# Kernel optimization log

Measured on AMD Instinct MI355X. Metric: run time of the kernel, lower is better.

Reference implementation:

```python
import jax, jax.numpy as jnp
import numpy as np

B, CIN, C, H, T = 8, 64, 64, 62, 400
S = 32              # StateSpaceLayer state_dim default
MID = max(1, C // 16)  # ChannelAttention reduction=16


def _dwconv(x, w, pad):
    # x [B,C,H,W], w [C,1,kh,kw], depthwise conv
    return jax.lax.conv_general_dilated(
        x, w, (1, 1), pad,
        dimension_numbers=('NCHW', 'OIHW', 'NCHW'),
        feature_group_count=x.shape[1])


def _pw(x, w):  # 1x1 conv, w [O,C]
    return jnp.einsum('bchw,oc->bohw', x, w)


def _bn(x, g, b):  # eval-mode BatchNorm with running mean=0, var=1 folded into affine
    return x * g[None, :, None, None] + b[None, :, None, None]


def _chan_attn(x, w1, w2):
    # AdaptiveAvg/MaxPool(1) -> shared MLP -> sigmoid gate
    avg = x.mean(axis=(2, 3))
    mx = x.max(axis=(2, 3))
    fc = lambda v: jax.nn.relu(v @ w1.T) @ w2.T  # Linear weights are [out,in]
    a = jax.nn.sigmoid(fc(avg) + fc(mx))
    return x * a[:, :, None, None]


def _spat_attn(x, w):
    avg = x.mean(axis=1, keepdims=True)
    mx = x.max(axis=1, keepdims=True)
    comb = jnp.concatenate([avg, mx], axis=1)  # [B,2,H,W]
    a = jax.nn.sigmoid(jax.lax.conv_general_dilated(
        comb, w, (1, 1), ((3, 3), (3, 3)),
        dimension_numbers=('NCHW', 'OIHW', 'NCHW')))
    return x * a


def _ssm(x, A, Bv, Cm, D, ln_g, ln_b):
    # Faithful to torch: raw reshape [B,C,H,T] -> [B*H, C, T] (row-major, same as torch)
    b, c, h, t = x.shape
    xs = x.reshape(b * h, c, t)
    seq = jnp.moveaxis(xs, 2, 0)  # [T, N, C]

    def step(state, inp):
        state = state @ A.T + Bv               # state = state A^T + B
        out = jax.nn.gelu(state @ Cm + inp * D, approximate=False)
        return state, out

    init = jnp.zeros((b * h, A.shape[0]), x.dtype)
    _, outs = jax.lax.scan(step, init, seq)    # outs [T, N, C]
    out = jnp.moveaxis(outs, 0, 2).reshape(b, c, h, t)
    out = x + out  # residual (dropout p=0)
    # LayerNorm over channel dim
    y = jnp.moveaxis(out, 1, -1)  # [B,H,T,C]
    mu = y.mean(-1, keepdims=True)
    var = ((y - mu) ** 2).mean(-1, keepdims=True)
    y = (y - mu) / jnp.sqrt(var + 1e-5) * ln_g + ln_b
    return jnp.moveaxis(y, -1, 1)


def _half(x, dwdw, dwpw, dwg, dwb, caw1, caw2, saw,
          d1dw, d1pw, d1g, d1b, A, Bv, Cm, D, lng, lnb):
    pad5 = ((2, 2), (2, 2))
    b1 = jax.nn.relu(_bn(_pw(_dwconv(x, dwdw[0], pad5), dwpw[0]), dwg[0], dwb[0]))
    b2 = jax.nn.relu(_bn(_pw(_dwconv(x, dwdw[1], pad5), dwpw[1]), dwg[1], dwb[1]))
    cb = b1 * _chan_attn(b1, caw1, caw2)       # note: x * ChannelAttention(x) as in source
    cb = _bn(_pw(_dwconv(cb, d1dw, ((0, 0), (1, 1))), d1pw), d1g, d1b)
    cb = jax.nn.sigmoid(cb)
    sb = jax.nn.sigmoid(b2 * _spat_attn(b2, saw))
    return _ssm(cb, A, Bv, Cm, D, lng, lnb) * sb


def setup_inputs() -> dict:
    key = jax.random.key(0)
    ks = jax.random.split(key, 16)
    n = lambda k, shp, s=0.1: jax.random.normal(k, shp, dtype=jnp.float32) * s
    return {
        'x': jax.random.normal(ks[0], (B, CIN, H, T), dtype=jnp.float32),
        'in_w': n(ks[1], (C, CIN)),
        'dw2d_dw': n(ks[2], (2, 2, C, 1, 5, 5)),
        'dw2d_pw': n(ks[3], (2, 2, C, C)),
        'dw2d_g': jnp.ones((2, 2, C), jnp.float32),
        'dw2d_b': jnp.zeros((2, 2, C), jnp.float32),
        'ca_w1': n(ks[4], (2, MID, C)),
        'ca_w2': n(ks[5], (2, C, MID)),
        'sa_w': n(ks[6], (2, 1, 2, 7, 7)),
        'dw1d_dw': n(ks[7], (2, C, 1, 1, 3)),
        'dw1d_pw': n(ks[8], (2, C, C)),
        'dw1d_g': jnp.ones((2, C), jnp.float32),
        'dw1d_b': jnp.zeros((2, C), jnp.float32),
        'ssm_A': n(ks[9], (2, S, S)),
        'ssm_B': n(ks[10], (2, S)),
        'ssm_C': n(ks[11], (2, S, C)),
        'ssm_D': n(ks[12], (2, C)),
        'ln_g': jnp.ones((2, C), jnp.float32),
        'ln_b': jnp.zeros((2, C), jnp.float32),
        'out_w': n(ks[13], (C, C)),
        'out_g': jnp.ones((C,), jnp.float32),
        'out_b': jnp.zeros((C,), jnp.float32),
    }


def reference(x, in_w, dw2d_dw, dw2d_pw, dw2d_g, dw2d_b, ca_w1, ca_w2, sa_w,
              dw1d_dw, dw1d_pw, dw1d_g, dw1d_b, ssm_A, ssm_B, ssm_C, ssm_D,
              ln_g, ln_b, out_w, out_g, out_b):
    h = _pw(x, in_w)
    o = _half(h, dw2d_dw[0], dw2d_pw[0], dw2d_g[0], dw2d_b[0], ca_w1[0], ca_w2[0],
              sa_w[0], dw1d_dw[0], dw1d_pw[0], dw1d_g[0], dw1d_b[0],
              ssm_A[0], ssm_B[0], ssm_C[0], ssm_D[0], ln_g[0], ln_b[0])
    o = o[..., ::-1]  # flip time axis
    o = _half(o, dw2d_dw[1], dw2d_pw[1], dw2d_g[1], dw2d_b[1], ca_w1[1], ca_w2[1],
              sa_w[1], dw1d_dw[1], dw1d_pw[1], dw1d_g[1], dw1d_b[1],
              ssm_A[1], ssm_B[1], ssm_C[1], ssm_D[1], ln_g[1], ln_b[1])
    o = o[..., ::-1]
    return jax.nn.relu(_bn(_pw(o, out_w), out_g, out_b))
```

## Files before the change

### kernel.cpp

```cpp
#include <hip/hip_runtime.h>
#include <math.h>

#define DI __device__ __forceinline__

constexpr int B_ = 8, C_ = 64, H_ = 62, T_ = 400, S_ = 32;
constexpr int HT   = H_ * T_;
constexpr int CHT  = C_ * HT;
constexpr int NPOS = B_ * HT;
constexpr int NTOT = B_ * CHT;

typedef __attribute__((ext_vector_type(8))) short short8;
typedef __attribute__((ext_vector_type(4))) float float4v;
typedef unsigned short bh;

DI float sigmoidf_(float x) { return 1.f / (1.f + expf(-x)); }
DI float gelu_(float x) { return 0.5f * x * (1.f + erff(x * 0.70710678118654752f)); }

template<int ACT> DI float act_(float v) {
  if (ACT == 1) return fmaxf(v, 0.f);
  if (ACT == 2) return sigmoidf_(v);
  return v;
}

DI bh f2b(float f) {
  unsigned int u = __float_as_uint(f);
  u += 0x7FFFu + ((u >> 16) & 1u);
  return (bh)(u >> 16);
}
DI float b2f(bh u) { return __uint_as_float(((unsigned int)u) << 16); }
DI unsigned int pk2(float a, float b) {
  return (unsigned int)f2b(a) | ((unsigned int)f2b(b) << 16);
}

__global__ __launch_bounds__(256) void prep(const float* __restrict__ in_w,
    const float* __restrict__ dwpw, const float* __restrict__ dwg,
    const float* __restrict__ d1pw, const float* __restrict__ d1g,
    const float* __restrict__ outw, const float* __restrict__ outg,
    bh* __restrict__ wf) {
  int idx = blockIdx.x * 256 + threadIdx.x;
  int lane = idx & 63, kc = (idx >> 6) & 1, w = (idx >> 7) & 3, slot = idx >> 9;
  const float* src; const float* g;
  switch (slot) {
    case 0: src = in_w;            g = nullptr;      break;
    case 1: src = dwpw + 0 * 4096; g = dwg + 0 * 64; break;
    case 2: src = dwpw + 1 * 4096; g = dwg + 1 * 64; break;
    case 3: src = d1pw + 0 * 4096; g = d1g + 0 * 64; break;
    case 4: src = dwpw + 2 * 4096; g = dwg + 2 * 64; break;
    case 5: src = dwpw + 3 * 4096; g = dwg + 3 * 64; break;
    case 6: src = d1pw + 1 * 4096; g = d1g + 1 * 64; break;
    default: src = outw;           g = outg;         break;
  }
  int o = w * 16 + (lane & 15);
  float gv = g ? g[o] : 1.f;
  unsigned int pack[4];
  #pragma unroll
  for (int h = 0; h < 4; ++h) {
    int c = kc * 32 + (lane >> 4) * 8 + h * 2;
    pack[h] = pk2(src[o * 64 + c] * gv, src[o * 64 + c + 1] * gv);
  }
  *(uint4*)&wf[idx * 8] = make_uint4(pack[0], pack[1], pack[2], pack[3]);
}

template<int ACT, bool REV, bool SPAT, bool DW13, bool INF32, bool OUTF32>
__global__ __launch_bounds__(256) void pwk(const void* __restrict__ in_,
    const bh* __restrict__ wf, const float* __restrict__ bb,
    const float* __restrict__ ac, const float* __restrict__ w3,
    void* __restrict__ out_, float* __restrict__ comb) {
  __shared__ bh Xb[128 * 72];
  const int tid = threadIdx.x;
  const int lane = tid & 63;
  const int wv = tid >> 6;
  const int p0 = blockIdx.x * 128;
  {
    const int ps = (tid & 31) * 4;
    const int cs = (tid >> 5) * 8;
    const int p4 = p0 + ps;
    const int b = p4 / HT, ht = p4 - b * HT;
    const int row = ht / T_, t0 = ht - row * T_;
    float xv[8][4];
    if constexpr (INF32) {
      const float* rp0 = (const float*)in_ + b * CHT + row * T_;
      #pragma unroll
      for (int cj = 0; cj < 8; ++cj) {
        const float* rp = rp0 + (cs + cj) * HT;
        if constexpr (REV) {
          float4 u = *(const float4*)&rp[T_ - 4 - t0];
          xv[cj][0] = u.w; xv[cj][1] = u.z; xv[cj][2] = u.y; xv[cj][3] = u.x;
        } else {
          float4 u = *(const float4*)&rp[t0];
          xv[cj][0] = u.x; xv[cj][1] = u.y; xv[cj][2] = u.z; xv[cj][3] = u.w;
        }
      }
    } else if constexpr (DW13) {
      const bh* rp0 = (const bh*)in_ + b * CHT + row * T_;
      #pragma unroll
      for (int cj = 0; cj < 8; ++cj) {
        const int c = cs + cj;
        const bh* rp = rp0 + c * HT;
        ushort4 u = *(const ushort4*)&rp[t0];
        float x0 = b2f(u.x), x1 = b2f(u.y), x2 = b2f(u.z), x3 = b2f(u.w);
        float xm = (t0 > 0)      ? b2f(rp[t0 - 1]) : 0.f;
        float xp = (t0 < T_ - 4) ? b2f(rp[t0 + 4]) : 0.f;
        float s0 = xm * xm, s1 = x0 * x0, s2 = x1 * x1;
        float s3 = x2 * x2, s4 = x3 * x3, s5 = xp * xp;
        float acv = ac[b * 64 + c];
        float c0 = w3[c * 3 + 0] * acv, c1 = w3[c * 3 + 1] * acv,
              c2 = w3[c * 3 + 2] * acv;
        xv[cj][0] = c0 * s0 + c1 * s1 + c2 * s2;
        xv[cj][1] = c0 * s1 + c1 * s2 + c2 * s3;
        xv[cj][2] = c0 * s2 + c1 * s3 + c2 * s4;
        xv[cj][3] = c0 * s3 + c1 * s4 + c2 * s5;
      }
    } else {
      const bh* rp0 = (const bh*)in_ + b * CHT + row * T_;
      #pragma unroll
      for (int cj = 0; cj < 8; ++cj) {
        const bh* rp = rp0 + (cs + cj) * HT;
        ushort4 u;
        if constexpr (REV) {
          u = *(const ushort4*)&rp[T_ - 4 - t0];
          xv[cj][0] = b2f(u.w); xv[cj][1] = b2f(u.z);
          xv[cj][2] = b2f(u.y); xv[cj][3] = b2f(u.x);
        } else {
          u = *(const ushort4*)&rp[t0];
          xv[cj][0] = b2f(u.x); xv[cj][1] = b2f(u.y);
          xv[cj][2] = b2f(u.z); xv[cj][3] = b2f(u.w);
        }
      }
    }
    #pragma unroll
    for (int pi = 0; pi < 4; ++pi) {
      int r = ps + pi;
      int col = cs ^ (((r >> 2) & 7) << 3);
      uint4 w4;
      w4.x = pk2(xv[0][pi], xv[1][pi]);
      w4.y = pk2(xv[2][pi], xv[3][pi]);
      w4.z = pk2(xv[4][pi], xv[5][pi]);
      w4.w = pk2(xv[6][pi], xv[7][pi]);
      *(uint4*)&Xb[r * 72 + col] = w4;
    }
  }
  short8 af0 = *(const short8*)(wf + ((wv * 2 + 0) * 64 + lane) * 8);
  short8 af1 = *(const short8*)(wf + ((wv * 2 + 1) * 64 + lane) * 8);
  const int m4 = (lane >> 4) * 4;
  float binit[4];
  #pragma unroll
  for (int j = 0; j < 4; ++j) binit[j] = bb ? bb[wv * 16 + m4 + j] : 0.f;
  __syncthreads();
  float4v acc[8];
  #pragma unroll
  for (int nt = 0; nt < 8; ++nt) { acc[nt][0] = acc[nt][1] = acc[nt][2] = acc[nt][3] = 0.f; }
  #pragma unroll
  for (int nt = 0; nt < 8; ++nt) {
    int r = nt * 16 + (lane & 15);
    int sw = ((r >> 2) & 7) << 3;
    int cb0 = ((lane >> 4) * 8) ^ sw;
    int cb1 = (32 + (lane >> 4) * 8) ^ sw;
    short8 b0 = *(const short8*)&Xb[r * 72 + cb0];
    short8 b1 = *(const short8*)&Xb[r * 72 + cb1];
    acc[nt] = __builtin_amdgcn_mfma_f32_16x16x32_bf16(af0, b0, acc[nt], 0, 0, 0);
    acc[nt] = __builtin_amdgcn_mfma_f32_16x16x32_bf16(af1, b1, acc[nt], 0, 0, 0);
  }
  float psum[8], pmaxv[8];
  #pragma unroll
  for (int nt = 0; nt < 8; ++nt) {
    int n = nt * 16 + (lane & 15);
    int p = p0 + n;
    int b = p / HT, ht = p - b * HT;
    float s = 0.f, m = -3.4e38f;
    if constexpr (OUTF32) {
      float* op = (float*)out_ + b * CHT + ht + (wv * 16 + m4) * HT;
      #pragma unroll
      for (int j = 0; j < 4; ++j) {
        float r = act_<ACT>(acc[nt][j] + binit[j]);
        op[j * HT] = r;
        if constexpr (SPAT) { s += r; m = fmaxf(m, r); }
      }
    } else {
      bh* op = (bh*)out_ + b * CHT + ht + (wv * 16 + m4) * HT;
      #pragma unroll
      for (int j = 0; j < 4; ++j) {
        float r = act_<ACT>(acc[nt][j] + binit[j]);
        op[j * HT] = f2b(r);
        if constexpr (SPAT) { s += r; m = fmaxf(m, r); }
      }
    }
    if constexpr (SPAT) {
      s += __shfl_xor(s, 16); s += __shfl_xor(s, 32);
      m = fmaxf(m, __shfl_xor(m, 16)); m = fmaxf(m, __shfl_xor(m, 32));
      psum[nt] = s; pmaxv[nt] = m;
    }
  }
  if constexpr (SPAT) {
    __shared__ float redS[4][128], redM[4][128];
    if (lane < 16) {
      #pragma unroll
      for (int nt = 0; nt < 8; ++nt) {
        redS[wv][nt * 16 + lane] = psum[nt];
        redM[wv][nt * 16 + lane] = pmaxv[nt];
      }
    }
    __syncthreads();
    if (tid < 128) {
      float s = redS[0][tid] + redS[1][tid] + redS[2][tid] + redS[3][tid];
      float m = fmaxf(fmaxf(redM[0][tid], redM[1][tid]),
                      fmaxf(redM[2][tid], redM[3][tid]));
      int pp = p0 + tid;
      int b2 = pp / HT, ht2 = pp - b2 * HT;
      comb[b2 * 2 * HT + ht2] = s * (1.f / 64.f);
      comb[b2 * 2 * HT + HT + ht2] = m;
    }
  }
}

__global__ __launch_bounds__(256) void dw5dual(const float* __restrict__ in,
    const float* __restrict__ w0_, const float* __restrict__ w1_,
    bh* __restrict__ out0, bh* __restrict__ out1) {
  const int bc = blockIdx.y;
  const int c = bc & 63;
  int task = blockIdx.x * 256 + threadIdx.x;
  if (task >= 62 * 25) return;
  int h = task / 25;
  int t0 = (task - h * 25) << 4;
  const float* base = in + (size_t)bc * HT;
  const float* wp0 = w0_ + c * 25;
  const float* wp1 = w1_ + c * 25;
  float acc0[16], acc1[16];
  #pragma unroll
  for (int j = 0; j < 16; ++j) { acc0[j] = 0.f; acc1[j] = 0.f; }
  const bool fast = (t0 >= 4) && (t0 <= 380);
  #pragma unroll 1
  for (int u = 0; u < 5; ++u) {
    int hh = h + u - 2;
    if (hh < 0 || hh >= H_) continue;
    const float* row = base + hh * T_;
    float win[24];
    if (fast) {
      #pragma unroll
      for (int j = 0; j < 6; ++j)
        *(float4*)&win[4 * j] = *(const float4*)&row[t0 - 4 + 4 * j];
    } else {
      #pragma unroll
      for (int k = 0; k < 24; ++k) {
        int tt = t0 - 4 + k;
        win[k] = (tt >= 0 && tt < T_) ? row[tt] : 0.f;
      }
    }
    #pragma unroll
    for (int v = 0; v < 5; ++v) {
      float wa = wp0[u * 5 + v];
      float wb = wp1[u * 5 + v];
      #pragma unroll
      for (int j = 0; j < 16; ++j) {
        float x = win[j + v + 2];
        acc0[j] += wa * x;
        acc1[j] += wb * x;
      }
    }
  }
  unsigned int pk0[8], pk1[8];
  #pragma unroll
  for (int j = 0; j < 8; ++j) {
    pk0[j] = pk2(acc0[2 * j], acc0[2 * j + 1]);
    pk1[j] = pk2(acc1[2 * j], acc1[2 * j + 1]);
  }
  bh* o0 = out0 + (size_t)bc * HT + h * T_ + t0;
  bh* o1 = out1 + (size_t)bc * HT + h * T_ + t0;
  *(uint4*)&o0[0] = make_uint4(pk0[0], pk0[1], pk0[2], pk0[3]);
  *(uint4*)&o0[8] = make_uint4(pk0[4], pk0[5], pk0[6], pk0[7]);
  *(uint4*)&o1[0] = make_uint4(pk1[0], pk1[1], pk1[2], pk1[3]);
  *(uint4*)&o1[8] = make_uint4(pk1[4], pk1[5], pk1[6], pk1[7]);
}

__global__ __launch_bounds__(256) void chanred(const bh* __restrict__ in,
    float* __restrict__ sum_, float* __restrict__ max_) {
  int bc = blockIdx.x >> 1, hf = blockIdx.x & 1;
  const bh* base = in + (size_t)bc * HT + hf * (HT / 2);
  float s = 0.f, m = -3.4e38f;
  for (int i = threadIdx.x * 2; i < HT / 2; i += 512) {
    ushort2 q = *(const ushort2*)&base[i];
    float v0 = b2f(q.x), v1 = b2f(q.y);
    s += v0 + v1; m = fmaxf(m, fmaxf(v0, v1));
  }
  #pragma unroll
  for (int off = 32; off > 0; off >>= 1) {
    s += __shfl_down(s, off);
    m = fmaxf(m, __shfl_down(m, off));
  }
  __shared__ float ss[4], sm[4];
  int wv = threadIdx.x >> 6;
  if ((threadIdx.x & 63) == 0) { ss[wv] = s; sm[wv] = m; }
  __syncthreads();
  if (threadIdx.x == 0) {
    float S = ss[0] + ss[1] + ss[2] + ss[3];
    float M = fmaxf(fmaxf(sm[0], sm[1]), fmaxf(sm[2], sm[3]));
    sum_[hf * 512 + bc] = S;
    max_[hf * 512 + bc] = M;
  }
}

__global__ __launch_bounds__(512) void cafc(const float* __restrict__ cs,
    const float* __restrict__ cm, const float* __restrict__ w1,
    const float* __restrict__ w2, float* __restrict__ ac) {
  __shared__ float sa[512], sx[512], hsum[8][4];
  int tid = threadIdx.x;
  sa[tid] = (cs[tid] + cs[512 + tid]) * (1.f / HT);
  sx[tid] = fmaxf(cm[tid], cm[512 + tid]);
  __syncthreads();
  if (tid < 32) {
    int b = tid >> 2, m = tid & 3;
    float s1 = 0.f, s2 = 0.f;
    #pragma unroll
    for (int cc = 0; cc < 64; ++cc) {
      float wv = w1[m * 64 + cc];
      s1 += sa[b * 64 + cc] * wv;
      s2 += sx[b * 64 + cc] * wv;
    }
    hsum[b][m] = fmaxf(s1, 0.f) + fmaxf(s2, 0.f);
  }
  __syncthreads();
  int b = tid >> 6, cc = tid & 63;
  float f = 0.f;
  #pragma unroll
  for (int m = 0; m < 4; ++m) f += hsum[b][m] * w2[cc * 4 + m];
  ac[tid] = sigmoidf_(f);
}

__global__ __launch_bounds__(256) void conv7(const float* __restrict__ comb,
    const float* __restrict__ w, float* __restrict__ as_) {
  __shared__ float sm[2][8][408];
  __shared__ float sw[98];
  const int b = blockIdx.x / 31, hp = blockIdx.x % 31;
  const int h0 = hp * 2;
  const float* cb0 = comb + b * 2 * HT;
  const int tid = threadIdx.x;
  if (tid < 98) sw[tid] = w[tid];
  for (int e = tid; e < 2 * 8 * 408; e += 256) {
    int ci = e / 3264, rem = e - ci * 3264;
    int r = rem / 408, tt = rem - r * 408;
    int hh = h0 - 3 + r, t = tt - 4;
    float v = 0.f;
    if (hh >= 0 && hh < H_ && t >= 0 && t < T_) v = cb0[ci * HT + hh * T_ + t];
    sm[ci][r][tt] = v;
  }
  __syncthreads();
  for (int o = tid; o < 800; o += 256) {
    int oh = o / 400, ot = o - oh * 400;
    float acc = 0.f;
    #pragma unroll
    for (int ci = 0; ci < 2; ++ci)
      #pragma unroll
      for (int u = 0; u < 7; ++u)
        #pragma unroll
        for (int v = 0; v < 7; ++v)
          acc += sw[ci * 49 + u * 7 + v] * sm[ci][oh + u][ot + v + 1];
    as_[b * HT + (h0 + oh) * T_ + ot] = sigmoidf_(acc);
  }
}

__global__ __launch_bounds__(1024) void ssmctA(const float* __restrict__ A_,
    const float* __restrict__ Bv_, float* __restrict__ Pg, float* __restrict__ qg) {
  const int hf = blockIdx.x;
  const float* A = A_ + hf * 1024;
  const float* Bv = Bv_ + hf * 32;
  __shared__ float Pbuf[2][32 * 33];
  __shared__ float qbuf[2][32];
  const int tid = threadIdx.x;
  float* Pc = Pbuf[0]; float* Pn = Pbuf[1];
  float* qc = qbuf[0]; float* qn = qbuf[1];
  Pc[(tid >> 5) * 33 + (tid & 31)] = A[tid];
  if (tid < 32) qc[tid] = Bv[tid];
  __syncthreads();
  for (int i = 0; i < 9; ++i) {
    Pg[(hf * 9 + i) * 1024 + tid] = Pc[(tid >> 5) * 33 + (tid & 31)];
    if (tid < 32) qg[(hf * 9 + i) * 32 + tid] = qc[tid];
    if (i == 8) break;
    const int r = tid >> 5, cc = tid & 31;
    float s0 = 0.f, s1 = 0.f, s2 = 0.f, s3 = 0.f;
    #pragma unroll
    for (int k = 0; k < 32; k += 4) {
      s0 += Pc[r * 33 + k + 0] * Pc[(k + 0) * 33 + cc];
      s1 += Pc[r * 33 + k + 1] * Pc[(k + 1) * 33 + cc];
      s2 += Pc[r * 33 + k + 2] * Pc[(k + 2) * 33 + cc];
      s3 += Pc[r * 33 + k + 3] * Pc[(k + 3) * 33 + cc];
    }
    float qv = 0.f;
    if (tid < 32) {
      float a0 = 0.f, a1 = 0.f;
      #pragma unroll
      for (int k = 0; k < 32; k += 2) {
        a0 += Pc[tid * 33 + k] * qc[k];
        a1 += Pc[tid * 33 + k + 1] * qc[k + 1];
      }
      qv = qc[tid] + a0 + a1;
    }
    Pn[r * 33 + cc] = s0 + s1 + s2 + s3;
    if (tid < 32) qn[tid] = qv;
    __syncthreads();
    float* tp = Pc; Pc = Pn; Pn = tp;
    float* tq = qc; qc = qn; qn = tq;
  }
}

__global__ __launch_bounds__(1024) void ssmctB(const float* __restrict__ Pg,
    const float* __restrict__ qg, const float* __restrict__ Cm_,
    float* __restrict__ ct) {
  const int hf = blockIdx.y;
  __shared__ float P[9][32][33];
  __shared__ float q[9][32];
  __shared__ float Cs[32 * 64];
  __shared__ float st[32][33];
  const int tid = threadIdx.x;
  #pragma unroll
  for (int i = 0; i < 9; ++i) {
    int rem = tid;
    P[i][rem >> 5][rem & 31] = Pg[(hf * 9 + i) * 1024 + rem];
  }
  if (tid < 9 * 32) q[tid >> 5][tid & 31] = qg[hf * 9 * 32 + tid];
  for (int e = tid; e < 2048; e += 1024) Cs[e] = Cm_[hf * 2048 + e];
  __syncthreads();
  const int grp = tid >> 5, j = tid & 31;
  const int tIdx = blockIdx.x * 32 + grp;
  const int n = tIdx + 1;
  float s = 0.f;
  #pragma unroll
  for (int i = 0; i < 9; ++i) {
    st[grp][j] = s;
    float a0 = q[i][j], a1 = 0.f;
    #pragma unroll
    for (int k = 0; k < 32; k += 2) {
      a0 += P[i][j][k] * st[grp][k];
      a1 += P[i][j][k + 1] * st[grp][k + 1];
    }
    s = ((n >> i) & 1) ? (a0 + a1) : s;
  }
  st[grp][j] = s;
  __syncthreads();
  #pragma unroll
  for (int e0 = 0; e0 < 2048; e0 += 1024) {
    int e = e0 + tid;
    int ts = e >> 6, c = e & 63;
    float a0 = 0.f, a1 = 0.f;
    #pragma unroll
    for (int k = 0; k < 32; k += 2) {
      a0 += st[ts][k] * Cs[k * 64 + c];
      a1 += st[ts][k + 1] * Cs[(k + 1) * 64 + c];
    }
    int tg = blockIdx.x * 32 + ts;
    if (tg < T_) ct[(hf * T_ + tg) * 64 + c] = a0 + a1;
  }
}

template<bool OUTF32>
__global__ __launch_bounds__(256) void k8(const bh* __restrict__ cb,
    const bh* __restrict__ b2, const float* __restrict__ as_,
    const float* __restrict__ ct, const float* __restrict__ D,
    const float* __restrict__ lng, const float* __restrict__ lnb,
    void* __restrict__ out, int rev) {
  __shared__ float ct_s[64 * 65];
  __shared__ float red[4 * 2 * 66];
  const int tid = threadIdx.x;
  const int pl = tid & 63, wg = tid >> 6;
  const int p0 = blockIdx.x * 64;
  #pragma unroll
  for (int k = 0; k < 16; ++k) {
    int idx = k * 256 + tid;
    int r = idx >> 6, c2 = idx & 63;
    int t = (p0 + r) % T_;
    ct_s[r * 65 + c2] = ct[t * C_ + c2];
  }
  const int p = p0 + pl;
  const int b = p / HT, ht = p - b * HT;
  const int h = ht / T_, t = ht - h * T_;
  __syncthreads();
  const bh* cbp = cb + b * CHT + ht;
  const bh* b2p = b2 + b * CHT + ht;
  float o[16];
  float sum = 0.f;
  #pragma unroll
  for (int i = 0; i < 16; ++i) {
    int c = wg * 16 + i;
    float xv = b2f(cbp[c * HT]);
    int c2 = (62 * c + h) & 63;
    float u = ct_s[pl * 65 + c2] + xv * D[c2];
    float v = xv + gelu_(u);
    o[i] = v; sum += v;
  }
  red[wg * 132 + pl] = sum;
  __syncthreads();
  float S = red[0 * 132 + pl] + red[1 * 132 + pl] + red[2 * 132 + pl] + red[3 * 132 + pl];
  float mu = S * (1.f / 64.f);
  float vp = 0.f;
  #pragma unroll
  for (int i = 0; i < 16; ++i) { float d = o[i] - mu; vp += d * d; }
  red[wg * 132 + 66 + pl] = vp;
  __syncthreads();
  float Q = red[0 * 132 + 66 + pl] + red[1 * 132 + 66 + pl] +
            red[2 * 132 + 66 + pl] + red[3 * 132 + 66 + pl];
  float rstd = rsqrtf(Q * (1.f / 64.f) + 1e-5f);
  float av = as_[p];
  int htw = rev ? (h * T_ + (T_ - 1 - t)) : ht;
  #pragma unroll
  for (int i = 0; i < 16; ++i) {
    int c = wg * 16 + i;
    float y = (o[i] - mu) * rstd * lng[c] + lnb[c];
    float bv = b2f(b2p[c * HT]);
    float r = y * sigmoidf_(bv * bv * av);
    if constexpr (OUTF32) ((float*)out)[b * CHT + htw + c * HT] = r;
    else                  ((bh*)out)[b * CHT + htw + c * HT] = f2b(r);
  }
}

extern "C" void kernel_launch(void* const* d_in, const int* in_sizes, int n_in,
                              void* d_out, int out_size, void* d_ws, size_t ws_size,
                              hipStream_t stream) {
  const float* x    = (const float*)d_in[0];
  const float* in_w = (const float*)d_in[1];
  const float* dwdw = (const float*)d_in[2];
  const float* dwpw = (const float*)d_in[3];
  const float* dwg  = (const float*)d_in[4];
  const float* dwb  = (const float*)d_in[5];
  const float* caw1 = (const float*)d_in[6];
  const float* caw2 = (const float*)d_in[7];
  const float* saw  = (const float*)d_in[8];
  const float* d1dw = (const float*)d_in[9];
  const float* d1pw = (const float*)d_in[10];
  const float* d1g  = (const float*)d_in[11];
  const float* d1b  = (const float*)d_in[12];
  const float* ssmA = (const float*)d_in[13];
  const float* ssmBv= (const float*)d_in[14];
  const float* ssmC = (const float*)d_in[15];
  const float* ssmD = (const float*)d_in[16];
  const float* lng  = (const float*)d_in[17];
  const float* lnb  = (const float*)d_in[18];
  const float* outw = (const float*)d_in[19];
  const float* outg = (const float*)d_in[20];
  const float* outb = (const float*)d_in[21];

  size_t need = (size_t)3 * NTOT * 4
              + (size_t)(2 * NPOS + NPOS + 1024 + 1024 + 512
                         + 2 * T_ * C_ + 2 * 9 * 1024 + 2 * 9 * 32) * 4
              + (size_t)8 * 4096 * 2;
  if (ws_size < need) return;

  float* W0f = (float*)d_ws;
  bh*    W0b = (bh*)W0f;
  bh*    Fa  = (bh*)(W0f + NTOT);
  bh*    Fb  = (bh*)(W0f + 2 * (size_t)NTOT);
  float* fbase = W0f + 3 * (size_t)NTOT;
  float* comb  = fbase;
  float* as_   = comb + 2 * NPOS;
  float* casum = as_ + NPOS;
  float* camax = casum + 1024;
  float* ac    = camax + 1024;
  float* ct    = ac + 512;
  float* Pg    = ct + 2 * T_ * C_;
  float* qg    = Pg + 2 * 9 * 1024;
  bh* Wbf = (bh*)(qg + 2 * 9 * 32);

  prep<<<16, 256, 0, stream>>>(in_w, dwpw, dwg, d1pw, d1g, outw, outg, Wbf);
  ssmctA<<<2, 1024, 0, stream>>>(ssmA, ssmBv, Pg, qg);
  ssmctB<<<dim3(13, 2), 1024, 0, stream>>>(Pg, qg, ssmC, ct);
  pwk<0, false, false, false, true, true><<<1550, 256, 0, stream>>>(
      x, Wbf + 0 * 4096, nullptr, nullptr, nullptr, W0f, nullptr);

  auto run_half = [&](int hf) {
    const float* dw0 = dwdw + (hf * 2 + 0) * C_ * 25;
    const float* dw1 = dwdw + (hf * 2 + 1) * C_ * 25;
    const float* b0  = dwb + (hf * 2 + 0) * C_;
    const float* b1w = dwb + (hf * 2 + 1) * C_;
    dw5dual<<<dim3(7, 512), 256, 0, stream>>>(W0f, dw0, dw1, Fa, Fb);
    pwk<1, false, false, false, false, false><<<1550, 256, 0, stream>>>(
        Fa, Wbf + (1 + hf * 3) * 4096, b0, nullptr, nullptr, W0b, nullptr);
    pwk<1, false, true, false, false, false><<<1550, 256, 0, stream>>>(
        Fb, Wbf + (2 + hf * 3) * 4096, b1w, nullptr, nullptr, Fa, comb);
    chanred<<<1024, 256, 0, stream>>>(W0b, casum, camax);
    cafc<<<1, 512, 0, stream>>>(casum, camax, caw1 + hf * 4 * 64, caw2 + hf * 64 * 4, ac);
    conv7<<<248, 256, 0, stream>>>(comb, saw + hf * 98, as_);
    pwk<2, false, false, true, false, false><<<1550, 256, 0, stream>>>(
        W0b, Wbf + (3 + hf * 3) * 4096, d1b + hf * C_, ac, d1dw + hf * C_ * 3,
        Fb, nullptr);
    if (hf == 0)
      k8<true><<<3100, 256, 0, stream>>>(Fb, Fa, as_, ct + hf * T_ * C_,
                                         ssmD + hf * C_, lng + hf * C_,
                                         lnb + hf * C_, W0f, 1);
    else
      k8<false><<<3100, 256, 0, stream>>>(Fb, Fa, as_, ct + hf * T_ * C_,
                                          ssmD + hf * C_, lng + hf * C_,
                                          lnb + hf * C_, W0b, 0);
  };

  run_half(0);
  run_half(1);
  pwk<1, true, false, false, false, true><<<1550, 256, 0, stream>>>(
      W0b, Wbf + 7 * 4096, outb, nullptr, nullptr, (float*)d_out, nullptr);
}
```

Measured before the change: 399.6 us.

## Fuse SSM/LayerNorm/gating epilogue into the final pointwise conv kernel

The separate k8 kernel (SSM output, GELU, residual, LayerNorm, spatial gating and optional time flip) is merged into the epilogue of the preceding MFMA pointwise conv. The conv output no longer round-trips through global memory as bf16 before being re-read. Workspace buffers are rotated so each half reads and writes distinct regions. This costs extra shared memory (a 128x65 float ct tile) and more register pressure in pwk, which may lower occupancy.

Measured after the change: 423.9 us. +6.1%, slower.

```diff
diff --git a/kernel.cpp b/kernel.cpp
--- a/kernel.cpp
+++ b/kernel.cpp
@@ -61,12 +61,19 @@
   *(uint4*)&wf[idx * 8] = make_uint4(pack[0], pack[1], pack[2], pack[3]);
 }
 
-template<int ACT, bool REV, bool SPAT, bool DW13, bool INF32, bool OUTF32>
+template<int ACT, bool REV, bool SPAT, bool DW13, bool INF32, bool OUTF32, bool K8F>
 __global__ __launch_bounds__(256) void pwk(const void* __restrict__ in_,
     const bh* __restrict__ wf, const float* __restrict__ bb,
     const float* __restrict__ ac, const float* __restrict__ w3,
-    void* __restrict__ out_, float* __restrict__ comb) {
-  __shared__ bh Xb[128 * 72];
+    void* __restrict__ out_, float* __restrict__ comb,
+    const bh* __restrict__ b2g, const float* __restrict__ asg,
+    const float* __restrict__ ctg, const float* __restrict__ Dg,
+    const float* __restrict__ lngg, const float* __restrict__ lnbg, int rev) {
+  constexpr int XB_B = 128 * 72 * 2;
+  constexpr int MAIN_B = K8F ? 128 * 65 * 4 : XB_B;
+  constexpr int RED_B = (K8F || SPAT) ? 4096 : 0;
+  __shared__ __align__(16) char smr_[MAIN_B + RED_B];
+  bh* Xb = (bh*)smr_;
   const int tid = threadIdx.x;
   const int lane = tid & 63;
   const int wv = tid >> 6;
@@ -161,54 +168,136 @@
     acc[nt] = __builtin_amdgcn_mfma_f32_16x16x32_bf16(af0, b0, acc[nt], 0, 0, 0);
     acc[nt] = __builtin_amdgcn_mfma_f32_16x16x32_bf16(af1, b1, acc[nt], 0, 0, 0);
   }
-  float psum[8], pmaxv[8];
-  #pragma unroll
-  for (int nt = 0; nt < 8; ++nt) {
-    int n = nt * 16 + (lane & 15);
-    int p = p0 + n;
-    int b = p / HT, ht = p - b * HT;
-    float s = 0.f, m = -3.4e38f;
-    if constexpr (OUTF32) {
-      float* op = (float*)out_ + b * CHT + ht + (wv * 16 + m4) * HT;
+  if constexpr (K8F) {
+    __syncthreads();
+    float* ctl  = (float*)smr_;
+    float* redA = (float*)(smr_ + MAIN_B);
+    float* redB = redA + 512;
+    for (int e = tid; e < 128 * 64; e += 256) {
+      int r = e >> 6, c2 = e & 63;
+      int p = p0 + r;
+      int ht = p % HT;
+      int t = ht % T_;
+      ctl[r * 65 + c2] = ctg[t * 64 + c2];
+    }
+    __syncthreads();
+    int offs[8], wof[8], h8[8];
+    float av8[8];
+    #pragma unroll
+    for (int nt = 0; nt < 8; ++nt) {
+      int p = p0 + nt * 16 + (lane & 15);
+      int b = p / HT, ht = p - b * HT;
+      int h = ht / T_, t = ht - h * T_;
+      offs[nt] = b * CHT + ht;
+      wof[nt] = b * CHT + (rev ? (h * T_ + T_ - 1 - t) : ht);
+      h8[nt] = h;
+      av8[nt] = asg[p];
+    }
+    #pragma unroll
+    for (int nt = 0; nt < 8; ++nt) {
+      int r = nt * 16 + (lane & 15);
       #pragma unroll
       for (int j = 0; j < 4; ++j) {
-        float r = act_<ACT>(acc[nt][j] + binit[j]);
-        op[j * HT] = r;
-        if constexpr (SPAT) { s += r; m = fmaxf(m, r); }
-      }
-    } else {
-      bh* op = (bh*)out_ + b * CHT + ht + (wv * 16 + m4) * HT;
+        int c = wv * 16 + m4 + j;
+        float cbv = act_<ACT>(acc[nt][j] + binit[j]);
+        int c2 = (h8[nt] - 2 * c) & 63;
+        float u = ctl[r * 65 + c2] + cbv * Dg[c2];
+        acc[nt][j] = cbv + gelu_(u);
+      }
+    }
+    #pragma unroll
+    for (int nt = 0; nt < 8; ++nt) {
+      float s = acc[nt][0] + acc[nt][1] + acc[nt][2] + acc[nt][3];
+      s += __shfl_xor(s, 16); s += __shfl_xor(s, 32);
+      if (lane < 16) redA[wv * 128 + nt * 16 + lane] = s;
+    }
+    __syncthreads();
+    float mu8[8];
+    #pragma unroll
+    for (int nt = 0; nt < 8; ++nt) {
+      int q = nt * 16 + (lane & 15);
+      mu8[nt] = (redA[q] + redA[128 + q] + redA[256 + q] + redA[384 + q])
+                * (1.f / 64.f);
+    }
+    #pragma unroll
+    for (int nt = 0; nt < 8; ++nt) {
+      float d0 = acc[nt][0] - mu8[nt], d1 = acc[nt][1] - mu8[nt];
+      float d2 = acc[nt][2] - mu8[nt], d3 = acc[nt][3] - mu8[nt];
+      float qv = d0 * d0 + d1 * d1 + d2 * d2 + d3 * d3;
+      qv += __shfl_xor(qv, 16); qv += __shfl_xor(qv, 32);
+      if (lane < 16) redB[wv * 128 + nt * 16 + lane] = qv;
+    }
+    __syncthreads();
+    float rstd8[8];
+    #pragma unroll
+    for (int nt = 0; nt < 8; ++nt) {
+      int q = nt * 16 + (lane & 15);
+      float Q = redB[q] + redB[128 + q] + redB[256 + q] + redB[384 + q];
+      rstd8[nt] = rsqrtf(Q * (1.f / 64.f) + 1e-5f);
+    }
+    #pragma unroll
+    for (int nt = 0; nt < 8; ++nt) {
       #pragma unroll
       for (int j = 0; j < 4; ++j) {
-        float r = act_<ACT>(acc[nt][j] + binit[j]);
-        op[j * HT] = f2b(r);
-        if constexpr (SPAT) { s += r; m = fmaxf(m, r); }
+        int c = wv * 16 + m4 + j;
+        float y = (acc[nt][j] - mu8[nt]) * rstd8[nt] * lngg[c] + lnbg[c];
+        float bv = b2f(b2g[offs[nt] + c * HT]);
+        float rr = y * sigmoidf_(bv * bv * av8[nt]);
+        if constexpr (OUTF32) ((float*)out_)[wof[nt] + c * HT] = rr;
+        else                  ((bh*)out_)[wof[nt] + c * HT] = f2b(rr);
+      }
+    }
+  } else {
+    float psum[8], pmaxv[8];
+    #pragma unroll
+    for (int nt = 0; nt < 8; ++nt) {
+      int n = nt * 16 + (lane & 15);
+      int p = p0 + n;
+      int b = p / HT, ht = p - b * HT;
+      float s = 0.f, m = -3.4e38f;
+      if constexpr (OUTF32) {
+        float* op = (float*)out_ + b * CHT + ht + (wv * 16 + m4) * HT;
+        #pragma unroll
+        for (int j = 0; j < 4; ++j) {
+          float r = act_<ACT>(acc[nt][j] + binit[j]);
+          op[j * HT] = r;
+          if constexpr (SPAT) { s += r; m = fmaxf(m, r); }
+        }
+      } else {
+        bh* op = (bh*)out_ + b * CHT + ht + (wv * 16 + m4) * HT;
+        #pragma unroll
+        for (int j = 0; j < 4; ++j) {
+          float r = act_<ACT>(acc[nt][j] + binit[j]);
+          op[j * HT] = f2b(r);
+          if constexpr (SPAT) { s += r; m = fmaxf(m, r); }
+        }
+      }
+      if constexpr (SPAT) {
+        s += __shfl_xor(s, 16); s += __shfl_xor(s, 32);
+        m = fmaxf(m, __shfl_xor(m, 16)); m = fmaxf(m, __shfl_xor(m, 32));
+        psum[nt] = s; pmaxv[nt] = m;
       }
     }
     if constexpr (SPAT) {
-      s += __shfl_xor(s, 16); s += __shfl_xor(s, 32);
-      m = fmaxf(m, __shfl_xor(m, 16)); m = fmaxf(m, __shfl_xor(m, 32));
-      psum[nt] = s; pmaxv[nt] = m;
-    }
-  }
-  if constexpr (SPAT) {
-    __shared__ float redS[4][128], redM[4][128];
-    if (lane < 16) {
-      #pragma unroll
-      for (int nt = 0; nt < 8; ++nt) {
-        redS[wv][nt * 16 + lane] = psum[nt];
-        redM[wv][nt * 16 + lane] = pmaxv[nt];
-      }
-    }
-    __syncthreads();
-    if (tid < 128) {
-      float s = redS[0][tid] + redS[1][tid] + redS[2][tid] + redS[3][tid];
-      float m = fmaxf(fmaxf(redM[0][tid], redM[1][tid]),
-                      fmaxf(redM[2][tid], redM[3][tid]));
-      int pp = p0 + tid;
-      int b2 = pp / HT, ht2 = pp - b2 * HT;
-      comb[b2 * 2 * HT + ht2] = s * (1.f / 64.f);
-      comb[b2 * 2 * HT + HT + ht2] = m;
+      float* redS = (float*)(smr_ + MAIN_B);
+      float* redM = redS + 512;
+      if (lane < 16) {
+        #pragma unroll
+        for (int nt = 0; nt < 8; ++nt) {
+          redS[wv * 128 + nt * 16 + lane] = psum[nt];
+          redM[wv * 128 + nt * 16 + lane] = pmaxv[nt];
+        }
+      }
+      __syncthreads();
+      if (tid < 128) {
+        float s = redS[tid] + redS[128 + tid] + redS[256 + tid] + redS[384 + tid];
+        float m = fmaxf(fmaxf(redM[tid], redM[128 + tid]),
+                        fmaxf(redM[256 + tid], redM[384 + tid]));
+        int pp = p0 + tid;
+        int b2i = pp / HT, ht2 = pp - b2i * HT;
+        comb[b2i * 2 * HT + ht2] = s * (1.f / 64.f);
+        comb[b2i * 2 * HT + HT + ht2] = m;
+      }
     }
   }
 }
@@ -448,66 +537,6 @@
     }
     int tg = blockIdx.x * 32 + ts;
     if (tg < T_) ct[(hf * T_ + tg) * 64 + c] = a0 + a1;
-  }
-}
-
-template<bool OUTF32>
-__global__ __launch_bounds__(256) void k8(const bh* __restrict__ cb,
-    const bh* __restrict__ b2, const float* __restrict__ as_,
-    const float* __restrict__ ct, const float* __restrict__ D,
-    const float* __restrict__ lng, const float* __restrict__ lnb,
-    void* __restrict__ out, int rev) {
-  __shared__ float ct_s[64 * 65];
-  __shared__ float red[4 * 2 * 66];
-  const int tid = threadIdx.x;
-  const int pl = tid & 63, wg = tid >> 6;
-  const int p0 = blockIdx.x * 64;
-  #pragma unroll
-  for (int k = 0; k < 16; ++k) {
-    int idx = k * 256 + tid;
-    int r = idx >> 6, c2 = idx & 63;
-    int t = (p0 + r) % T_;
-    ct_s[r * 65 + c2] = ct[t * C_ + c2];
-  }
-  const int p = p0 + pl;
-  const int b = p / HT, ht = p - b * HT;
-  const int h = ht / T_, t = ht - h * T_;
-  __syncthreads();
-  const bh* cbp = cb + b * CHT + ht;
-  const bh* b2p = b2 + b * CHT + ht;
-  float o[16];
-  float sum = 0.f;
-  #pragma unroll
-  for (int i = 0; i < 16; ++i) {
-    int c = wg * 16 + i;
-    float xv = b2f(cbp[c * HT]);
-    int c2 = (62 * c + h) & 63;
-    float u = ct_s[pl * 65 + c2] + xv * D[c2];
-    float v = xv + gelu_(u);
-    o[i] = v; sum += v;
-  }
-  red[wg * 132 + pl] = sum;
-  __syncthreads();
-  float S = red[0 * 132 + pl] + red[1 * 132 + pl] + red[2 * 132 + pl] + red[3 * 132 + pl];
-  float mu = S * (1.f / 64.f);
-  float vp = 0.f;
-  #pragma unroll
-  for (int i = 0; i < 16; ++i) { float d = o[i] - mu; vp += d * d; }
-  red[wg * 132 + 66 + pl] = vp;
-  __syncthreads();
-  float Q = red[0 * 132 + 66 + pl] + red[1 * 132 + 66 + pl] +
-            red[2 * 132 + 66 + pl] + red[3 * 132 + 66 + pl];
-  float rstd = rsqrtf(Q * (1.f / 64.f) + 1e-5f);
-  float av = as_[p];
-  int htw = rev ? (h * T_ + (T_ - 1 - t)) : ht;
-  #pragma unroll
-  for (int i = 0; i < 16; ++i) {
-    int c = wg * 16 + i;
-    float y = (o[i] - mu) * rstd * lng[c] + lnb[c];
-    float bv = b2f(b2p[c * HT]);
-    float r = y * sigmoidf_(bv * bv * av);
-    if constexpr (OUTF32) ((float*)out)[b * CHT + htw + c * HT] = r;
-    else                  ((bh*)out)[b * CHT + htw + c * HT] = f2b(r);
   }
 }
 
@@ -543,11 +572,11 @@
               + (size_t)8 * 4096 * 2;
   if (ws_size < need) return;
 
-  float* W0f = (float*)d_ws;
-  bh*    W0b = (bh*)W0f;
-  bh*    Fa  = (bh*)(W0f + NTOT);
-  bh*    Fb  = (bh*)(W0f + 2 * (size_t)NTOT);
-  float* fbase = W0f + 3 * (size_t)NTOT;
+  float* R0f = (float*)d_ws;
+  float* R1f = R0f + NTOT;
+  float* R2f = R1f + NTOT;
+  bh* R0b = (bh*)R0f; bh* R1b = (bh*)R1f; bh* R2b = (bh*)R2f;
+  float* fbase = R0f + 3 * (size_t)NTOT;
   float* comb  = fbase;
   float* as_   = comb + 2 * NPOS;
   float* casum = as_ + NPOS;
@@ -561,37 +590,41 @@
   prep<<<16, 256, 0, stream>>>(in_w, dwpw, dwg, d1pw, d1g, outw, outg, Wbf);
   ssmctA<<<2, 1024, 0, stream>>>(ssmA, ssmBv, Pg, qg);
   ssmctB<<<dim3(13, 2), 1024, 0, stream>>>(Pg, qg, ssmC, ct);
-  pwk<0, false, false, false, true, true><<<1550, 256, 0, stream>>>(
-      x, Wbf + 0 * 4096, nullptr, nullptr, nullptr, W0f, nullptr);
-
-  auto run_half = [&](int hf) {
+  pwk<0, false, false, false, true, true, false><<<1550, 256, 0, stream>>>(
+      x, Wbf + 0 * 4096, nullptr, nullptr, nullptr, R0f, nullptr,
+      nullptr, nullptr, nullptr, nullptr, nullptr, nullptr, 0);
+
+  auto run_half = [&](int hf, float* Xf, bh* D0, bh* D1, bh* B1, bh* B2,
+                      void* Xout, bool outf32) {
     const float* dw0 = dwdw + (hf * 2 + 0) * C_ * 25;
     const float* dw1 = dwdw + (hf * 2 + 1) * C_ * 25;
     const float* b0  = dwb + (hf * 2 + 0) * C_;
     const float* b1w = dwb + (hf * 2 + 1) * C_;
-    dw5dual<<<dim3(7, 512), 256, 0, stream>>>(W0f, dw0, dw1, Fa, Fb);
-    pwk<1, false, false, false, false, false><<<1550, 256, 0, stream>>>(
-        Fa, Wbf + (1 + hf * 3) * 4096, b0, nullptr, nullptr, W0b, nullptr);
-    pwk<1, false, true, false, false, false><<<1550, 256, 0, stream>>>(
-        Fb, Wbf + (2 + hf * 3) * 4096, b1w, nullptr, nullptr, Fa, comb);
-    chanred<<<1024, 256, 0, stream>>>(W0b, casum, camax);
+    dw5dual<<<dim3(7, 512), 256, 0, stream>>>(Xf, dw0, dw1, D0, D1);
+    pwk<1, false, false, false, false, false, false><<<1550, 256, 0, stream>>>(
+        D0, Wbf + (1 + hf * 3) * 4096, b0, nullptr, nullptr, B1, nullptr,
+        nullptr, nullptr, nullptr, nullptr, nullptr, nullptr, 0);
+    pwk<1, false, true, false, false, false, false><<<1550, 256, 0, stream>>>(
+        D1, Wbf + (2 + hf * 3) * 4096, b1w, nullptr, nullptr, B2, comb,
+        nullptr, nullptr, nullptr, nullptr, nullptr, nullptr, 0);
+    chanred<<<1024, 256, 0, stream>>>(B1, casum, camax);
     cafc<<<1, 512, 0, stream>>>(casum, camax, caw1 + hf * 4 * 64, caw2 + hf * 64 * 4, ac);
     conv7<<<248, 256, 0, stream>>>(comb, saw + hf * 98, as_);
-    pwk<2, false, false, true, false, false><<<1550, 256, 0, stream>>>(
-        W0b, Wbf + (3 + hf * 3) * 4096, d1b + hf * C_, ac, d1dw + hf * C_ * 3,
-        Fb, nullptr);
-    if (hf == 0)
-      k8<true><<<3100, 256, 0, stream>>>(Fb, Fa, as_, ct + hf * T_ * C_,
-                                         ssmD + hf * C_, lng + hf * C_,
-                                         lnb + hf * C_, W0f, 1);
+    if (outf32)
+      pwk<2, false, false, true, false, true, true><<<1550, 256, 0, stream>>>(
+          B1, Wbf + (3 + hf * 3) * 4096, d1b + hf * C_, ac, d1dw + hf * C_ * 3,
+          Xout, nullptr, B2, as_, ct + hf * T_ * C_, ssmD + hf * C_,
+          lng + hf * C_, lnb + hf * C_, hf == 0 ? 1 : 0);
     else
-      k8<false><<<3100, 256, 0, stream>>>(Fb, Fa, as_, ct + hf * T_ * C_,
-                                          ssmD + hf * C_, lng + hf * C_,
-                                          lnb + hf * C_, W0b, 0);
+      pwk<2, false, false, true, false, false, true><<<1550, 256, 0, stream>>>(
+          B1, Wbf + (3 + hf * 3) * 4096, d1b + hf * C_, ac, d1dw + hf * C_ * 3,
+          Xout, nullptr, B2, as_, ct + hf * T_ * C_, ssmD + hf * C_,
+          lng + hf * C_, lnb + hf * C_, hf == 0 ? 1 : 0);
   };
 
-  run_half(0);
-  run_half(1);
-  pwk<1, true, false, false, false, true><<<1550, 256, 0, stream>>>(
-      W0b, Wbf + 7 * 4096, outb, nullptr, nullptr, (float*)d_out, nullptr);
-}
+  run_half(0, R0f, R1b, R2b, R0b, R1b, (void*)R2f, true);
+  run_half(1, R2f, R0b, R1b, R2b, R0b, (void*)R1b, false);
+  pwk<1, true, false, false, false, true, false><<<1550, 256, 0, stream>>>(
+      R1b, Wbf + 7 * 4096, outb, nullptr, nullptr, (float*)d_out, nullptr,
+      nullptr, nullptr, nullptr, nullptr, nullptr, nullptr, 0);
+}
```
